# Performance work log

Measured on AMD Instinct MI355X. Metric: run time of the kernel, lower is better.

Reference implementation:

```python
import jax, jax.numpy as jnp
import numpy as np
import math

D = 768; H = 8; HD = D // H; T = 1024; V = 32000; M = 10
BLOCK = 128          # flex-attention block size (sliding_window_num_blocks granularity)
TAU = 1.0            # gumbel_temp
MAXC = 10            # max middle-block visits == scan length
EPS = 1e-6
IFP = 0.95           # initial_forward_prob

def rms(x):
    return x * jax.lax.rsqrt(jnp.mean(x * x, axis=-1, keepdims=True) + EPS)

def make_rope(t):
    # Rotary.__init__: dim//4 real inv freqs + dim//4 zeros -> cos/sin of shape [t, HD//2]
    inv = (1.0 / 1024) ** jnp.linspace(0.0, 1.0, HD // 4)
    inv = jnp.concatenate([inv, jnp.zeros(HD // 4)])
    th = jnp.arange(t, dtype=jnp.float32)[:, None] * inv[None, :]
    return jnp.cos(th), jnp.sin(th)

def rope(x, cos, sin):
    # x: [1,T,H,HD]
    c = cos[None, :, None, :]; s = sin[None, :, None, :]
    x1, x2 = jnp.split(x, 2, axis=-1)
    return jnp.concatenate([x1 * c + x2 * s, -x1 * s + x2 * c], axis=-1)

def attn(x, ve, wq, wk, wv, wo, lam, cos, sin, mask):
    q = (x @ wq.T).reshape(1, T, H, HD)
    k = (x @ wk.T).reshape(1, T, H, HD)
    v = (x @ wv.T).reshape(1, T, H, HD)
    if ve is not None:
        v = lam[0] * v + lam[1] * ve.reshape(1, T, H, HD)
    else:
        v = lam[0] * v
    q = rope(rms(q), cos, sin); k = rope(rms(k), cos, sin)
    sc = jnp.einsum('bthd,bshd->bhts', q, k) * (1.0 / math.sqrt(HD))
    sc = jnp.where(mask, sc, -1e30)
    y = jnp.einsum('bhts,bshd->bthd', jax.nn.softmax(sc, axis=-1), v).reshape(1, T, D)
    return y @ wo.T

def mlp(x, fc, pr):
    return jnp.square(jax.nn.relu(x @ fc.T)) @ pr.T

def fwd(tokens, embed_w, ve_w, lm_head_w,
        in_wq, in_wk, in_wv, in_wo, in_attn_lam, in_fc, in_pr, in_lam,
        mid_wq, mid_wk, mid_wv, mid_wo, mid_attn_lam, mid_fc, mid_pr, router_w, router_b,
        out_wq, out_wk, out_wv, out_wo, out_attn_lam, out_fc, out_pr, out_lam,
        gumbel_u, window_blocks, max_block_count):
    cos, sin = make_rope(T)
    qi = jnp.arange(T)
    mask = ((qi[:, None] >= qi[None, :]) &
            ((qi[:, None] // BLOCK - qi[None, :] // BLOCK) < window_blocks))[None, None]
    x = rms(embed_w[tokens][None])     # norm(embed(inputs))
    x0 = x
    ve = ve_w[tokens][None]            # X=1 value embedding, reused for output block
    # ---- input FixedBlock ----
    h = in_lam[0] * x + in_lam[1] * x0
    h = h + attn(rms(h), ve, in_wq, in_wk, in_wv, in_wo, in_attn_lam, cos, sin, mask)
    h = h + mlp(rms(h), in_fc, in_pr)
    # ---- middle routing loop (fixed-length scan, masked once exited) ----
    g = -jnp.log(-jnp.log(gumbel_u + 1e-10) + 1e-10)  # [MAXC, M+1] gumbel noise
    mbc = jnp.float32(max_block_count)
    def step(carry, gi):
        x, cur, done, cnt = carry
        y = x + attn(rms(x), None, mid_wq[cur], mid_wk[cur], mid_wv[cur], mid_wo[cur],
                     mid_attn_lam[cur], cos, sin, mask)
        y = y + mlp(rms(y), mid_fc[cur], mid_pr[cur])
        feat = jnp.concatenate([y.mean(axis=1), jnp.stack([cnt, mbc])[None]], axis=-1)  # [1, D+2]
        logits = feat @ router_w[cur].T + router_b[cur]                                  # [1, M+1]
        route = jax.nn.softmax((logits + gi[None]) / TAU, axis=-1)
        nxt = jnp.argmax(route[0]).astype(jnp.int32)
        new_cnt = cnt + 1.0
        exit_now = (nxt == M) | (new_cnt >= mbc)
        x = jnp.where(done, x, y)
        cnt = jnp.where(done, cnt, new_cnt)
        new_done = done | exit_now
        cur = jnp.where(new_done, cur, nxt)
        return (x, cur, new_done, cnt), None
    init = (h, jnp.int32(0), jnp.bool_(False), jnp.float32(0.0))
    (x, _, _, _), _ = jax.lax.scan(step, init, g)
    # ---- output FixedBlock ----
    y = out_lam[0] * x + out_lam[1] * x0
    y = y + attn(rms(y), ve, out_wq, out_wk, out_wv, out_wo, out_attn_lam, cos, sin, mask)
    y = y + mlp(rms(y), out_fc, out_pr)
    logits = rms(y) @ lm_head_w.T
    return 30.0 * jnp.tanh(logits / 30.0)

def setup_inputs() -> dict:
    key = jax.random.key(0)
    ks = iter(jax.random.split(key, 64))
    def w(*s, std=0.02):
        return (std * jax.random.normal(next(ks), s)).astype(jnp.float32)
    rb = np.full((M, M + 1), math.log((1.0 - IFP) / M), dtype=np.float32)
    for i in range(M):
        rb[i, min(i + 1, M)] = math.log(IFP)
    inp = {
        'tokens': jax.random.randint(next(ks), (T,), 0, V, dtype=jnp.int32),
        'embed_w': w(V, D), 've_w': w(V, D), 'lm_head_w': w(V, D),
        'in_wq': w(D, D), 'in_wk': w(D, D), 'in_wv': w(D, D), 'in_wo': w(D, D),
        'in_attn_lam': jnp.array([0.5, 0.5], jnp.float32),
        'in_fc': w(4 * D, D), 'in_pr': w(D, 4 * D),
        'in_lam': jnp.array([1.0, 0.0], jnp.float32),
        'mid_wq': w(M, D, D), 'mid_wk': w(M, D, D), 'mid_wv': w(M, D, D), 'mid_wo': w(M, D, D),
        'mid_attn_lam': jnp.tile(jnp.array([0.5, 0.5], jnp.float32), (M, 1)),
        'mid_fc': w(M, 4 * D, D), 'mid_pr': w(M, D, 4 * D),
        'router_w': w(M, M + 1, D + 2, std=0.001),
        'router_b': jnp.asarray(rb),
        'out_wq': w(D, D), 'out_wk': w(D, D), 'out_wv': w(D, D), 'out_wo': w(D, D),
        'out_attn_lam': jnp.array([0.5, 0.5], jnp.float32),
        'out_fc': w(4 * D, D), 'out_pr': w(D, 4 * D),
        'out_lam': jnp.array([1.0, 0.0], jnp.float32),
        'gumbel_u': jax.random.uniform(next(ks), (MAXC, M + 1), dtype=jnp.float32),
        'window_blocks': 4,
        'max_block_count': MAXC,
    }
    return inp

def reference(tokens, embed_w, ve_w, lm_head_w,
              in_wq, in_wk, in_wv, in_wo, in_attn_lam, in_fc, in_pr, in_lam,
              mid_wq, mid_wk, mid_wv, mid_wo, mid_attn_lam, mid_fc, mid_pr, router_w, router_b,
              out_wq, out_wk, out_wv, out_wo, out_attn_lam, out_fc, out_pr, out_lam,
              gumbel_u, window_blocks, max_block_count):
    return fwd(tokens, embed_w, ve_w, lm_head_w,
               in_wq, in_wk, in_wv, in_wo, in_attn_lam, in_fc, in_pr, in_lam,
               mid_wq, mid_wk, mid_wv, mid_wo, mid_attn_lam, mid_fc, mid_pr, router_w, router_b,
               out_wq, out_wk, out_wv, out_wo, out_attn_lam, out_fc, out_pr, out_lam,
               gumbel_u, window_blocks, max_block_count)
```

## Files before the change

### kernel.cpp

```cpp
#include <hip/hip_runtime.h>
#include <hip/hip_bf16.h>

namespace {

constexpr int cT   = 1024;
constexpr int cD   = 768;
constexpr int cH   = 8;
constexpr int cHD  = 96;
constexpr int cM   = 10;
constexpr int cDff = 3072;
constexpr int cV   = 32000;
constexpr int cTD  = cT * cD;
constexpr float cEps = 1e-6f;

constexpr long oWQ = 0;
constexpr long oWK = 589824;
constexpr long oWV = 2L * 589824;
constexpr long oWO = 3L * 589824;
constexpr long oFC = 4L * 589824;
constexpr long oPR = 4L * 589824 + 2359296;
constexpr long cWTOT = 4L * 589824 + 2L * 2359296;
constexpr int cConvBlocks = (int)(cWTOT / 8 / 256);

typedef __attribute__((ext_vector_type(8))) short short8;
typedef __attribute__((ext_vector_type(4))) float f32x4;

__device__ inline short bf16r(float f) {
  union { float f; unsigned u; } x{f};
  unsigned r = (x.u + 0x7FFF + ((x.u >> 16) & 1)) >> 16;
  return (short)r;
}

__device__ inline float bf2f(short s) {
  union { unsigned u; float f; } x;
  x.u = ((unsigned)(unsigned short)s) << 16;
  return x.f;
}


__global__ void init_state_k(int* cur, int* done, float* cnt) {
  if (threadIdx.x == 0) { *cur = 0; *done = 0; *cnt = 0.0f; }
}

__global__ void rope_pre_k(float* __restrict__ cosb, float* __restrict__ sinb) {
  int idx = blockIdx.x * blockDim.x + threadIdx.x;
  if (idx >= cT * 48) return;
  int t = idx / 48, j = idx % 48;
  float th = 0.0f;
  if (j < 24) th = (float)t * powf(1.0f / 1024.0f, (float)j / 23.0f);
  cosb[idx] = cosf(th);
  sinb[idx] = sinf(th);
}

__global__ __launch_bounds__(256) void embed_rms_k(const int* __restrict__ tok,
    const float* __restrict__ ew, const float* __restrict__ vw,
    float* __restrict__ x0, float* __restrict__ ve) {
  int t = blockIdx.x;
  int tk = tok[t];
  const float* er = ew + (size_t)tk * cD;
  const float* vr = vw + (size_t)tk * cD;
  __shared__ float red[256];
  float s = 0.f;
  for (int d = threadIdx.x; d < cD; d += 256) { float e = er[d]; s += e * e; }
  red[threadIdx.x] = s; __syncthreads();
  for (int st = 128; st; st >>= 1) { if (threadIdx.x < st) red[threadIdx.x] += red[threadIdx.x + st]; __syncthreads(); }
  float sc = rsqrtf(red[0] / cD + cEps);
  for (int d = threadIdx.x; d < cD; d += 256) {
    x0[(size_t)t * cD + d] = er[d] * sc;
    ve[(size_t)t * cD + d] = vr[d];
  }
}

__global__ __launch_bounds__(256) void rms_rows_bf(const float* __restrict__ in,
    short* __restrict__ out, const int* done) {
  if (done && *done) return;
  int t = blockIdx.x;
  const float* r = in + (size_t)t * cD;
  __shared__ float red[256];
  float s = 0.f;
  for (int d = threadIdx.x; d < cD; d += 256) { float v = r[d]; s += v * v; }
  red[threadIdx.x] = s; __syncthreads();
  for (int st = 128; st; st >>= 1) { if (threadIdx.x < st) red[threadIdx.x] += red[threadIdx.x + st]; __syncthreads(); }
  float sc = rsqrtf(red[0] / cD + cEps);
  short* o = out + (size_t)t * cD;
  for (int d = threadIdx.x; d < cD; d += 256) o[d] = bf16r(r[d] * sc);
}

__global__ void axpy_lam_k(const float* __restrict__ lam, const float* __restrict__ a,
                           const float* __restrict__ b, float* __restrict__ o, int n) {
  int i = blockIdx.x * 256 + threadIdx.x;
  if (i < n) o[i] = lam[0] * a[i] + lam[1] * b[i];
}


__global__ __launch_bounds__(256) void layer_pre_k(const float* __restrict__ s0,
    const float* __restrict__ s1, const float* __restrict__ s2, const float* __restrict__ s3,
    const float* __restrict__ s4, const float* __restrict__ s5, short* __restrict__ dst,
    const int* __restrict__ cur, const int* __restrict__ done,
    const float* __restrict__ xin, short* __restrict__ xnbf, float* __restrict__ rsum) {
  if (done && *done) return;
  const int b = blockIdx.x;
  if (b < cConvBlocks) {
    long e = ((long)b * 256 + threadIdx.x) * 8;
    long cu = cur ? (long)(*cur) : 0L;
    const float* src;
    if (e < oWK)      src = s0 + cu * 589824  + e;
    else if (e < oWV) src = s1 + cu * 589824  + (e - oWK);
    else if (e < oWO) src = s2 + cu * 589824  + (e - oWV);
    else if (e < oFC) src = s3 + cu * 589824  + (e - oWO);
    else if (e < oPR) src = s4 + cu * 2359296 + (e - oFC);
    else              src = s5 + cu * 2359296 + (e - oPR);
    float4 a0 = *(const float4*)src;
    float4 a1 = *(const float4*)(src + 4);
    short8 sv;
    sv[0]=bf16r(a0.x); sv[1]=bf16r(a0.y); sv[2]=bf16r(a0.z); sv[3]=bf16r(a0.w);
    sv[4]=bf16r(a1.x); sv[5]=bf16r(a1.y); sv[6]=bf16r(a1.z); sv[7]=bf16r(a1.w);
    *(short8*)(dst + e) = sv;
  } else {
    const int t = b - cConvBlocks;
    const float* r = xin + (size_t)t * cD;
    __shared__ float red[256];
    float s = 0.f;
    for (int d = threadIdx.x; d < cD; d += 256) { float v = r[d]; s += v * v; }
    red[threadIdx.x] = s; __syncthreads();
    for (int st = 128; st; st >>= 1) { if (threadIdx.x < st) red[threadIdx.x] += red[threadIdx.x + st]; __syncthreads(); }
    float sc = rsqrtf(red[0] / cD + cEps);
    short* o = xnbf + (size_t)t * cD;
    for (int d = threadIdx.x; d < cD; d += 256) o[d] = bf16r(r[d] * sc);
    if (threadIdx.x == 0) rsum[t] = 0.f;
  }
}

__global__ __launch_bounds__(256) void conv1_k(const float* __restrict__ src,
    short* __restrict__ dst, long nchunk) {
  long i = (long)blockIdx.x * 256 + threadIdx.x;
  if (i >= nchunk) return;
  long e = i * 8;
  float4 a0 = *(const float4*)(src + e);
  float4 a1 = *(const float4*)(src + e + 4);
  short8 sv;
  sv[0]=bf16r(a0.x); sv[1]=bf16r(a0.y); sv[2]=bf16r(a0.z); sv[3]=bf16r(a0.w);
  sv[4]=bf16r(a1.x); sv[5]=bf16r(a1.y); sv[6]=bf16r(a1.z); sv[7]=bf16r(a1.w);
  *(short8*)(dst + e) = sv;
}


__global__ __launch_bounds__(256) void qkv_k(const short* __restrict__ A,
    const short* __restrict__ Wb,
    short* __restrict__ qo, short* __restrict__ ko, short* __restrict__ vo,
    const int* __restrict__ done, const float* __restrict__ lamb,
    const int* __restrict__ cur, const float* __restrict__ vep,
    const float* __restrict__ cosb, const float* __restrict__ sinb) {
  if (done && *done) return;
  const int z = blockIdx.z;
  const short* W = Wb + (long)z * 589824L;
  const int h  = blockIdx.x;
  const int bm = blockIdx.y * 64;
  __shared__ short As[2][64][40];
  __shared__ short Bs[2][96][40];
  const int tid = threadIdx.x;
  const int w = tid >> 6, lane = tid & 63;
  const int fr = lane & 15, fg = lane >> 4;
  const int ar = tid >> 2, ac2 = (tid & 3) << 3;
  const int br1 = (256 + tid) >> 2, bc1 = ((256 + tid) & 3) << 3;

  short8 aN, bN0, bN1;
  aN  = *(const short8*)(A + (size_t)(bm + ar) * cD + ac2);
  bN0 = *(const short8*)(W + (size_t)(h * cHD + ar) * cD + ac2);
  if (tid < 128) bN1 = *(const short8*)(W + (size_t)(h * cHD + br1) * cD + bc1);
  *(short8*)&As[0][ar][ac2] = aN;
  *(short8*)&Bs[0][ar][ac2] = bN0;
  if (tid < 128) *(short8*)&Bs[0][br1][bc1] = bN1;
  __syncthreads();

  f32x4 acc[6] = {};
  int cb = 0;
  for (int kt = 0; kt < cD; kt += 32) {
    const int ktn = kt + 32;
    const bool hn = ktn < cD;
    if (hn) {
      aN  = *(const short8*)(A + (size_t)(bm + ar) * cD + ktn + ac2);
      bN0 = *(const short8*)(W + (size_t)(h * cHD + ar) * cD + ktn + ac2);
      if (tid < 128) bN1 = *(const short8*)(W + (size_t)(h * cHD + br1) * cD + ktn + bc1);
    }
    short8 af = *(const short8*)&As[cb][w * 16 + fr][fg * 8];
#pragma unroll
    for (int n = 0; n < 6; ++n) {
      short8 bf = *(const short8*)&Bs[cb][n * 16 + fr][fg * 8];
      acc[n] = __builtin_amdgcn_mfma_f32_16x16x32_bf16(af, bf, acc[n], 0, 0, 0);
    }
    if (hn) {
      *(short8*)&As[cb ^ 1][ar][ac2] = aN;
      *(short8*)&Bs[cb ^ 1][ar][ac2] = bN0;
      if (tid < 128) *(short8*)&Bs[cb ^ 1][br1][bc1] = bN1;
    }
    __syncthreads();
    cb ^= 1;
  }

  const int t0 = bm + w * 16 + fg * 4;
  if (z < 2) {
    float scl[4];
#pragma unroll
    for (int r = 0; r < 4; ++r) {
      float s = 0.f;
#pragma unroll
      for (int n = 0; n < 6; ++n) s += acc[n][r] * acc[n][r];
#pragma unroll
      for (int mm = 1; mm < 16; mm <<= 1) s += __shfl_xor(s, mm, 64);
      scl[r] = rsqrtf(s * (1.0f / 96.0f) + cEps);
    }
    short* C = (z == 0 ? qo : ko);
#pragma unroll
    for (int r = 0; r < 4; ++r) {
      int t = t0 + r;
      short* orow = C + (size_t)t * cD + h * cHD;
#pragma unroll
      for (int n = 0; n < 3; ++n) {
        int j = n * 16 + fr;
        float c = cosb[t * 48 + j], sn = sinb[t * 48 + j];
        float x1 = acc[n][r] * scl[r], x2 = acc[n + 3][r] * scl[r];
        orow[j]      = bf16r(x1 * c + x2 * sn);
        orow[j + 48] = bf16r(-x1 * sn + x2 * c);
      }
    }
  } else {
    int cu = cur ? *cur : 0;
    float l0 = lamb[2 * cu], l1 = lamb[2 * cu + 1];
#pragma unroll
    for (int r = 0; r < 4; ++r) {
      int t = t0 + r;
#pragma unroll
      for (int n = 0; n < 6; ++n) {
        float val = l0 * acc[n][r];
        if (vep) val += l1 * vep[(size_t)t * cD + h * cHD + n * 16 + fr];
        vo[(size_t)t * cD + h * cHD + n * 16 + fr] = bf16r(val);
      }
    }
  }
}


__global__ __launch_bounds__(256) void attn_f(const short* __restrict__ q,
    const short* __restrict__ k, const short* __restrict__ v, short* __restrict__ o,
    const int* __restrict__ wbp, const int* done) {
  if (done && *done) return;
  const int qb = blockIdx.x;
  const int h  = blockIdx.y;
  const int q0 = qb * 64;
  const int qb128 = q0 >> 7;
  const int wb = *wbp;
  int kb_lo = qb128 - wb + 1; if (kb_lo < 0) kb_lo = 0;

  __shared__ short Ksh[128][136];
  __shared__ short Vt[96][136];

  const int tid  = threadIdx.x;
  const int w    = tid >> 6;
  const int lane = tid & 63;
  const int fr   = lane & 15;
  const int fg   = lane >> 4;

  short8 qf[3];
  {
    const short* qrow = q + (size_t)(q0 + w * 16 + fr) * cD + h * cHD;
#pragma unroll
    for (int ks = 0; ks < 3; ++ks) qf[ks] = *(const short8*)(qrow + ks * 32 + fg * 8);
  }

  f32x4 accO[6] = {};
  float mrun[4], lrun[4];
#pragma unroll
  for (int r = 0; r < 4; ++r) { mrun[r] = -1e30f; lrun[r] = 0.f; }

  for (int kb = kb_lo; kb <= qb128; ++kb) {
    __syncthreads();
    const int key0 = kb * 128;
#pragma unroll
    for (int c = 0; c < 6; ++c) {
      int idx = c * 256 + tid;
      int row = idx / 12, colc = (idx % 12) * 8;
      *(short8*)&Ksh[row][colc] =
          *(const short8*)(k + (size_t)(key0 + row) * cD + h * cHD + colc);
      short8 vv = *(const short8*)(v + (size_t)(key0 + row) * cD + h * cHD + colc);
#pragma unroll
      for (int i = 0; i < 8; ++i) Vt[colc + i][row] = vv[i];
    }
    __syncthreads();

    f32x4 s[8];
#pragma unroll
    for (int n = 0; n < 8; ++n) s[n] = (f32x4){0.f, 0.f, 0.f, 0.f};
#pragma unroll
    for (int ks = 0; ks < 3; ++ks) {
#pragma unroll
      for (int n = 0; n < 8; ++n) {
        short8 kf = *(const short8*)&Ksh[n * 16 + fr][ks * 32 + fg * 8];
        s[n] = __builtin_amdgcn_mfma_f32_16x16x32_bf16(qf[ks], kf, s[n], 0, 0, 0);
      }
    }

    float pmax[4] = {-1e30f, -1e30f, -1e30f, -1e30f};
#pragma unroll
    for (int n = 0; n < 8; ++n)
#pragma unroll
      for (int r = 0; r < 4; ++r) {
        float val = s[n][r] * 0.10206207261596577f;
        int key  = key0 + n * 16 + fr;
        int qrow = q0 + w * 16 + fg * 4 + r;
        if (key > qrow) val = -1e30f;
        s[n][r] = val;
        pmax[r] = fmaxf(pmax[r], val);
      }
#pragma unroll
    for (int mm = 1; mm < 16; mm <<= 1)
#pragma unroll
      for (int r = 0; r < 4; ++r) pmax[r] = fmaxf(pmax[r], __shfl_xor(pmax[r], mm, 64));
    float alpha[4], psum[4];
#pragma unroll
    for (int r = 0; r < 4; ++r) {
      float mn = fmaxf(mrun[r], pmax[r]);
      alpha[r] = __expf(mrun[r] - mn);
      mrun[r] = mn;
      psum[r] = 0.f;
    }
#pragma unroll
    for (int n = 0; n < 8; ++n)
#pragma unroll
      for (int r = 0; r < 4; ++r) {
        float p = __expf(s[n][r] - mrun[r]);
        s[n][r] = p;
        psum[r] += p;
      }
#pragma unroll
    for (int mm = 1; mm < 16; mm <<= 1)
#pragma unroll
      for (int r = 0; r < 4; ++r) psum[r] += __shfl_xor(psum[r], mm, 64);
#pragma unroll
    for (int r = 0; r < 4; ++r) lrun[r] = lrun[r] * alpha[r] + psum[r];
#pragma unroll
    for (int n = 0; n < 6; ++n) {
      f32x4 t = accO[n];
#pragma unroll
      for (int r = 0; r < 4; ++r) t[r] *= alpha[r];
      accO[n] = t;
    }

    __syncthreads();
#pragma unroll
    for (int n = 0; n < 8; ++n)
#pragma unroll
      for (int r = 0; r < 4; ++r)
        Ksh[w * 16 + fg * 4 + r][n * 16 + fr] = bf16r(s[n][r]);
    __syncthreads();

#pragma unroll
    for (int ks = 0; ks < 4; ++ks) {
      short8 pf = *(const short8*)&Ksh[w * 16 + fr][ks * 32 + fg * 8];
#pragma unroll
      for (int n = 0; n < 6; ++n) {
        short8 vf = *(const short8*)&Vt[n * 16 + fr][ks * 32 + fg * 8];
        accO[n] = __builtin_amdgcn_mfma_f32_16x16x32_bf16(pf, vf, accO[n], 0, 0, 0);
      }
    }
  }

#pragma unroll
  for (int r = 0; r < 4; ++r) {
    float inv = 1.0f / lrun[r];
    int t = q0 + w * 16 + fg * 4 + r;
#pragma unroll
    for (int n = 0; n < 6; ++n)
      o[(size_t)t * cD + h * cHD + n * 16 + fr] = bf16r(accO[n][r] * inv);
  }
}


template <int EPI, typename OT>
__global__ __launch_bounds__(256) void gemm64_k(const short* __restrict__ A,
    const short* __restrict__ W, OT* __restrict__ C, const int* __restrict__ done,
    const float* __restrict__ res, float* __restrict__ rsum, int ld, int kn, int N) {
  if (done && *done) return;
  const int bm = blockIdx.y * 64;
  const int bn = blockIdx.x * 64;
  const int k0 = blockIdx.z * kn;
  __shared__ short As[2][64][40];
  __shared__ short Bs[2][64][40];
  const int tid = threadIdx.x;
  const int wid = tid >> 6, lane = tid & 63;
  const int wr = wid >> 1, wc = wid & 1;
  const int fr = lane & 15, fg = lane >> 4;
  const int ar = tid >> 2, ac = (tid & 3) << 3;

  short8 aN = *(const short8*)(A + (size_t)(bm + ar) * ld + k0 + ac);
  short8 bN = *(const short8*)(W + (size_t)(bn + ar) * ld + k0 + ac);
  *(short8*)&As[0][ar][ac] = aN;
  *(short8*)&Bs[0][ar][ac] = bN;
  __syncthreads();

  f32x4 acc[2][2] = {};
  int cb = 0;
  for (int kt = 0; kt < kn; kt += 32) {
    const int ktn = kt + 32;
    const bool hn = ktn < kn;
    if (hn) {
      aN = *(const short8*)(A + (size_t)(bm + ar) * ld + k0 + ktn + ac);
      bN = *(const short8*)(W + (size_t)(bn + ar) * ld + k0 + ktn + ac);
    }
    short8 af[2], bfv[2];
#pragma unroll
    for (int m = 0; m < 2; ++m) af[m] = *(const short8*)&As[cb][wr * 32 + m * 16 + fr][fg * 8];
#pragma unroll
    for (int n = 0; n < 2; ++n) bfv[n] = *(const short8*)&Bs[cb][wc * 32 + n * 16 + fr][fg * 8];
#pragma unroll
    for (int m = 0; m < 2; ++m)
#pragma unroll
      for (int n = 0; n < 2; ++n)
        acc[m][n] = __builtin_amdgcn_mfma_f32_16x16x32_bf16(af[m], bfv[n], acc[m][n], 0, 0, 0);
    if (hn) {
      *(short8*)&As[cb ^ 1][ar][ac] = aN;
      *(short8*)&Bs[cb ^ 1][ar][ac] = bN;
    }
    __syncthreads();
    cb ^= 1;
  }
#pragma unroll
  for (int m = 0; m < 2; ++m)
#pragma unroll
    for (int r = 0; r < 4; ++r) {
      const int row = bm + wr * 32 + m * 16 + fg * 4 + r;
      float p = 0.f;
#pragma unroll
      for (int n = 0; n < 2; ++n) {
        const int col = bn + wc * 32 + n * 16 + fr;
        float val = acc[m][n][r];
        if constexpr (EPI == 1) {
          val += res[(size_t)row * N + col];
          C[(size_t)row * N + col] = val;
          p += val * val;
        } else {
          C[(size_t)blockIdx.z * cTD + (size_t)row * N + col] = (OT)bf16r(val);
        }
      }
      if constexpr (EPI == 1) {
#pragma unroll
        for (int mm = 1; mm < 16; mm <<= 1) p += __shfl_xor(p, mm, 64);
        if (fr == 0) atomicAdd(&rsum[row], p);
      }
    }
}


__global__ __launch_bounds__(256) void mgemm_fc_k(const float* __restrict__ Ay,
    const float* __restrict__ rsum, const short* __restrict__ W, short* __restrict__ C,
    const int* __restrict__ done, int K, int N) {
  if (done && *done) return;
  const int bm = blockIdx.y * 64;
  const int bn = blockIdx.x * 128;
  __shared__ short As[2][64][40];
  __shared__ short Bs[2][128][40];
  const int tid = threadIdx.x;
  const int wid = tid >> 6, lane = tid & 63;
  const int wr = wid >> 1, wc = wid & 1;
  const int fr = lane & 15, fg = lane >> 4;
  const int ar = tid >> 2, ac = (tid & 3) << 3;
  const int br1 = (256 + tid) >> 2, bc1 = ((256 + tid) & 3) << 3;

  const float ascl = rsqrtf(rsum[bm + ar] * (1.0f / cD) + cEps);
  const float* arow = Ay + (size_t)(bm + ar) * K;

  auto loadA = [&](int kt) -> short8 {
    float4 a0 = *(const float4*)(arow + kt + ac);
    float4 a1 = *(const float4*)(arow + kt + ac + 4);
    short8 sv;
    sv[0]=bf16r(a0.x*ascl); sv[1]=bf16r(a0.y*ascl); sv[2]=bf16r(a0.z*ascl); sv[3]=bf16r(a0.w*ascl);
    sv[4]=bf16r(a1.x*ascl); sv[5]=bf16r(a1.y*ascl); sv[6]=bf16r(a1.z*ascl); sv[7]=bf16r(a1.w*ascl);
    return sv;
  };

  short8 aN, bN0, bN1;
  aN  = loadA(0);
  bN0 = *(const short8*)(W + (size_t)(bn + ar) * K + ac);
  bN1 = *(const short8*)(W + (size_t)(bn + br1) * K + bc1);
  *(short8*)&As[0][ar][ac] = aN;
  *(short8*)&Bs[0][ar][ac] = bN0;
  *(short8*)&Bs[0][br1][bc1] = bN1;
  __syncthreads();

  f32x4 acc[2][4] = {};
  int cb = 0;
  for (int kt = 0; kt < K; kt += 32) {
    const int ktn = kt + 32;
    const bool hn = ktn < K;
    if (hn) {
      aN  = loadA(ktn);
      bN0 = *(const short8*)(W + (size_t)(bn + ar) * K + ktn + ac);
      bN1 = *(const short8*)(W + (size_t)(bn + br1) * K + ktn + bc1);
    }
    short8 af[2], bfv[4];
#pragma unroll
    for (int m = 0; m < 2; ++m) af[m] = *(const short8*)&As[cb][wr * 32 + m * 16 + fr][fg * 8];
#pragma unroll
    for (int n = 0; n < 4; ++n) bfv[n] = *(const short8*)&Bs[cb][wc * 64 + n * 16 + fr][fg * 8];
#pragma unroll
    for (int m = 0; m < 2; ++m)
#pragma unroll
      for (int n = 0; n < 4; ++n)
        acc[m][n] = __builtin_amdgcn_mfma_f32_16x16x32_bf16(af[m], bfv[n], acc[m][n], 0, 0, 0);
    if (hn) {
      *(short8*)&As[cb ^ 1][ar][ac] = aN;
      *(short8*)&Bs[cb ^ 1][ar][ac] = bN0;
      *(short8*)&Bs[cb ^ 1][br1][bc1] = bN1;
    }
    __syncthreads();
    cb ^= 1;
  }
#pragma unroll
  for (int m = 0; m < 2; ++m)
#pragma unroll
    for (int n = 0; n < 4; ++n)
#pragma unroll
      for (int r = 0; r < 4; ++r) {
        int row = bm + wr * 32 + m * 16 + fg * 4 + r;
        int col = bn + wc * 64 + n * 16 + fr;
        float val = acc[m][n][r];
        val = fmaxf(val, 0.f); val = val * val;
        C[(size_t)row * N + col] = bf16r(val);
      }
}


__global__ __launch_bounds__(256) void reduce_k(const short* __restrict__ pb,
    float* __restrict__ y, float* __restrict__ x, float* __restrict__ feat,
    const int* done) {
  if (done && *done) return;
  __shared__ float red[256];
  const int d = blockIdx.x * 32 + (threadIdx.x & 31);
  const int tc = threadIdx.x >> 5;
  float s = 0.f;
  for (int t = tc * 128; t < tc * 128 + 128; ++t) {
    size_t i = (size_t)t * cD + d;
    float v = y[i];
#pragma unroll
    for (int z = 0; z < 4; ++z) v += bf2f(pb[(size_t)z * cTD + i]);
    y[i] = v;
    if (x) x[i] = v;
    s += v;
  }
  if (feat) {
    red[threadIdx.x] = s; __syncthreads();
    if (threadIdx.x < 32) {
      float tot = 0.f;
#pragma unroll
      for (int c = 0; c < 8; ++c) tot += red[c * 32 + threadIdx.x];
      feat[d] = tot * (1.0f / cT);
    }
  }
}


__global__ void router_step_k(const float* __restrict__ feat, const float* __restrict__ rw,
    const float* __restrict__ rb, const float* __restrict__ gu, int iter,
    const int* __restrict__ mbcp, int* cur, int* done, float* cnt) {
  if (*done) return;
  __shared__ float lg[cM + 1];
  const int tid = threadIdx.x;
  const int c = *cur;
  const float mbc = (float)(*mbcp);
  const float cn = *cnt;
  for (int j = 0; j < cM + 1; ++j) {
    const float* w = rw + ((size_t)c * (cM + 1) + j) * (cD + 2);
    float s = 0.f;
    for (int d = tid; d < cD; d += 64) s += feat[d] * w[d];
#pragma unroll
    for (int mm = 32; mm; mm >>= 1) s += __shfl_xor(s, mm, 64);
    if (tid == 0) {
      s += cn * w[cD] + mbc * w[cD + 1] + rb[c * (cM + 1) + j];
      float u = gu[iter * (cM + 1) + j];
      float inner = -logf(u + 1e-10f) + 1e-10f;
      lg[j] = s - logf(inner);
    }
  }
  __syncthreads();
  if (tid == 0) {
    int nxt = 0; float best = lg[0];
    for (int j = 1; j < cM + 1; ++j) if (lg[j] > best) { best = lg[j]; nxt = j; }
    float nc = cn + 1.0f;
    int ex = (nxt == cM) || (nc >= mbc);
    *cnt = nc;
    if (ex) *done = 1; else *cur = nxt;
  }
}


__global__ __launch_bounds__(512) void gemm_lm_k(const short* __restrict__ A,
    const short* __restrict__ W, float* __restrict__ C) {
  const int nwg = (cV / 128) * (cT / 256);
  const int cpx = nwg / 8;
  const int swz = (blockIdx.x % 8) * cpx + blockIdx.x / 8;
  const int bm = (swz % 4) * 256;
  const int bn = (swz / 4) * 128;
  __shared__ short As[2][256][40];
  __shared__ short Bs[2][128][40];
  const int tid = threadIdx.x;
  const int wid = tid >> 6, lane = tid & 63;
  const int wr = wid >> 1, wc = wid & 1;
  const int fr = lane & 15, fg = lane >> 4;
  const int ar0 = tid >> 2, ac0 = (tid & 3) << 3;
  const int ar1 = (512 + tid) >> 2, ac1 = ((512 + tid) & 3) << 3;

  short8 aN0, aN1, bN;
  aN0 = *(const short8*)(A + (size_t)(bm + ar0) * cD + ac0);
  aN1 = *(const short8*)(A + (size_t)(bm + ar1) * cD + ac1);
  bN  = *(const short8*)(W + (size_t)(bn + ar0) * cD + ac0);
  *(short8*)&As[0][ar0][ac0] = aN0;
  *(short8*)&As[0][ar1][ac1] = aN1;
  *(short8*)&Bs[0][ar0][ac0] = bN;
  __syncthreads();

  f32x4 acc[4][4] = {};
  int cb = 0;
  for (int kt = 0; kt < cD; kt += 32) {
    const int ktn = kt + 32;
    const bool hn = ktn < cD;
    if (hn) {
      aN0 = *(const short8*)(A + (size_t)(bm + ar0) * cD + ktn + ac0);
      aN1 = *(const short8*)(A + (size_t)(bm + ar1) * cD + ktn + ac1);
      bN  = *(const short8*)(W + (size_t)(bn + ar0) * cD + ktn + ac0);
    }
    short8 af[4], bfv[4];
#pragma unroll
    for (int m = 0; m < 4; ++m) af[m] = *(const short8*)&As[cb][wr * 64 + m * 16 + fr][fg * 8];
#pragma unroll
    for (int n = 0; n < 4; ++n) bfv[n] = *(const short8*)&Bs[cb][wc * 64 + n * 16 + fr][fg * 8];
#pragma unroll
    for (int m = 0; m < 4; ++m)
#pragma unroll
      for (int n = 0; n < 4; ++n)
        acc[m][n] = __builtin_amdgcn_mfma_f32_16x16x32_bf16(af[m], bfv[n], acc[m][n], 0, 0, 0);
    if (hn) {
      *(short8*)&As[cb ^ 1][ar0][ac0] = aN0;
      *(short8*)&As[cb ^ 1][ar1][ac1] = aN1;
      *(short8*)&Bs[cb ^ 1][ar0][ac0] = bN;
    }
    __syncthreads();
    cb ^= 1;
  }
#pragma unroll
  for (int m = 0; m < 4; ++m)
#pragma unroll
    for (int n = 0; n < 4; ++n)
#pragma unroll
      for (int r = 0; r < 4; ++r) {
        int row = bm + wr * 64 + m * 16 + fg * 4 + r;
        int col = bn + wc * 64 + n * 16 + fr;
        C[(size_t)row * cV + col] = 30.f * tanhf(acc[m][n][r] * (1.f / 30.f));
      }
}

}


extern "C" void kernel_launch(void* const* d_in, const int* in_sizes, int n_in,
                              void* d_out, int out_size, void* d_ws, size_t ws_size,
                              hipStream_t stream) {
  const int*   tokens    = (const int*)d_in[0];
  const float* embed_w   = (const float*)d_in[1];
  const float* ve_w      = (const float*)d_in[2];
  const float* lm_head_w = (const float*)d_in[3];
  const float* in_wq  = (const float*)d_in[4];
  const float* in_wk  = (const float*)d_in[5];
  const float* in_wv  = (const float*)d_in[6];
  const float* in_wo  = (const float*)d_in[7];
  const float* in_al  = (const float*)d_in[8];
  const float* in_fc  = (const float*)d_in[9];
  const float* in_pr  = (const float*)d_in[10];
  const float* in_lam = (const float*)d_in[11];
  const float* mid_wq = (const float*)d_in[12];
  const float* mid_wk = (const float*)d_in[13];
  const float* mid_wv = (const float*)d_in[14];
  const float* mid_wo = (const float*)d_in[15];
  const float* mid_al = (const float*)d_in[16];
  const float* mid_fc = (const float*)d_in[17];
  const float* mid_pr = (const float*)d_in[18];
  const float* router_w = (const float*)d_in[19];
  const float* router_b = (const float*)d_in[20];
  const float* out_wq = (const float*)d_in[21];
  const float* out_wk = (const float*)d_in[22];
  const float* out_wv = (const float*)d_in[23];
  const float* out_wo = (const float*)d_in[24];
  const float* out_al = (const float*)d_in[25];
  const float* out_fc = (const float*)d_in[26];
  const float* out_pr = (const float*)d_in[27];
  const float* out_lam = (const float*)d_in[28];
  const float* gumbel_u = (const float*)d_in[29];
  const int*   wbp  = (const int*)d_in[30];
  const int*   mbcp = (const int*)d_in[31];
  float* outp = (float*)d_out;

  float* ws = (float*)d_ws;
  float* xb   = ws;
  float* x0b  = xb  + cTD;
  float* veb  = x0b + cTD;
  float* yb   = veb + cTD;
  float* cosb = yb  + cTD;
  float* sinb = cosb + cT * 48;
  float* rsum = sinb + cT * 48;
  float* feat = rsum + 1024;
  int*   curp  = (int*)(feat + 784);
  int*   donep = curp + 1;
  float* cntp  = (float*)(curp + 2);
  short* xnbf  = (short*)(feat + 784 + 8);
  short* aobf  = xnbf + cTD;
  short* qbf   = aobf + cTD;
  short* kbf   = qbf  + cTD;
  short* vbf   = kbf  + cTD;
  short* pbuf  = aobf;
  short* hidbf = vbf  + cTD;
  short* wbf   = hidbf + (size_t)cT * cDff;

  const dim3 gPre(cConvBlocks + cT, 1, 1);
  const dim3 gQKV(cH, cT / 64, 3);
  const dim3 gWO(cD / 64, cT / 64, 1);
  const dim3 gPR(cD / 64, cT / 64, 4);
  const dim3 gFF(cDff / 128, cT / 64, 1);
  const dim3 gLM(1000, 1, 1);
  const dim3 gAttn(cT / 64, cH, 1);
  const int gRed = cD / 32;
  const long lmChunks = (long)cV * cD / 8;
  const int gConvLM = (int)(lmChunks / 256);

  auto layer = [&](const float* wq, const float* wk, const float* wv, const float* wo,
                   const float* alam, const float* fc, const float* pr,
                   const int* cur, const int* done,
                   float* xin, float* yout, const float* vept,
                   float* xcom, float* featp) {
    layer_pre_k<<<gPre, 256, 0, stream>>>(wq, wk, wv, wo, fc, pr, wbf, cur, done,
                                          xin, xnbf, rsum);
    qkv_k<<<gQKV, 256, 0, stream>>>(xnbf, wbf, qbf, kbf, vbf, done, alam, cur, vept,
                                    cosb, sinb);
    attn_f<<<gAttn, 256, 0, stream>>>(qbf, kbf, vbf, aobf, wbp, done);
    gemm64_k<1, float><<<gWO, 256, 0, stream>>>(aobf, wbf + oWO, yout, done, xin, rsum,
                                                cD, cD, cD);
    mgemm_fc_k<<<gFF, 256, 0, stream>>>(yout, rsum, wbf + oFC, hidbf, done, cD, cDff);
    gemm64_k<4, short><<<gPR, 256, 0, stream>>>(hidbf, wbf + oPR, pbuf, done, nullptr,
                                                nullptr, cDff, cDff / 4, cD);
    reduce_k<<<gRed, 256, 0, stream>>>(pbuf, yout, xcom, featp, done);
  };

  init_state_k<<<1, 64, 0, stream>>>(curp, donep, cntp);
  rope_pre_k<<<(cT * 48 + 255) / 256, 256, 0, stream>>>(cosb, sinb);
  embed_rms_k<<<cT, 256, 0, stream>>>(tokens, embed_w, ve_w, x0b, veb);

  axpy_lam_k<<<cTD / 256, 256, 0, stream>>>(in_lam, x0b, x0b, xb, cTD);
  layer(in_wq, in_wk, in_wv, in_wo, in_al, in_fc, in_pr, nullptr, nullptr,
        xb, xb, veb, nullptr, nullptr);

  for (int it = 0; it < cM; ++it) {
    layer(mid_wq, mid_wk, mid_wv, mid_wo, mid_al, mid_fc, mid_pr,
          curp, donep, xb, yb, nullptr, xb, feat);
    router_step_k<<<1, 64, 0, stream>>>(feat, router_w, router_b, gumbel_u, it, mbcp,
                                        curp, donep, cntp);
  }

  axpy_lam_k<<<cTD / 256, 256, 0, stream>>>(out_lam, xb, x0b, xb, cTD);
  layer(out_wq, out_wk, out_wv, out_wo, out_al, out_fc, out_pr, nullptr, nullptr,
        xb, xb, veb, nullptr, nullptr);

  conv1_k<<<gConvLM, 256, 0, stream>>>(lm_head_w, wbf, lmChunks);
  rms_rows_bf<<<cT, 256, 0, stream>>>(xb, xnbf, nullptr);
  gemm_lm_k<<<gLM, 512, 0, stream>>>(xnbf, wbf, outp);
}
```

Baseline: 2.631 ms.

## Pre-convert all layer and LM-head weights to bf16 once, halve attention tile

A single up-front kernel converts every weight set to bf16 into slots of one workspace buffer: all ten middle-block slots, the input and output blocks, and the LM head. The GEMM kernels then read the right slot through a device-side block index and stride. This removes the per-layer fp32-to-bf16 weight conversion and the separate LM-head conversion, at the cost of converting middle-block weights that an early router exit never uses, and it requires a larger workspace (otherwise it falls back to the old path). Separately, the attention kernel now handles 32 queries per block with 128 threads instead of 64 queries with 256, doubling the block count to improve parallelism.

```diff
diff --git a/kernel.cpp b/kernel.cpp
--- a/kernel.cpp
+++ b/kernel.cpp
@@ -21,6 +21,8 @@
 constexpr long oPR = 4L * 589824 + 2359296;
 constexpr long cWTOT = 4L * 589824 + 2L * 2359296;
 constexpr int cConvBlocks = (int)(cWTOT / 8 / 256);
+constexpr long cLM  = (long)cV * cD;
+constexpr long cALL = 12L * cWTOT + cLM;
 
 typedef __attribute__((ext_vector_type(8))) short short8;
 typedef __attribute__((ext_vector_type(4))) float f32x4;
@@ -86,12 +88,67 @@
   for (int d = threadIdx.x; d < cD; d += 256) o[d] = bf16r(r[d] * sc);
 }
 
+__global__ __launch_bounds__(256) void rms_pre_k(const float* __restrict__ in,
+    short* __restrict__ out, float* __restrict__ rsum, const int* done) {
+  if (done && *done) return;
+  int t = blockIdx.x;
+  const float* r = in + (size_t)t * cD;
+  __shared__ float red[256];
+  float s = 0.f;
+  for (int d = threadIdx.x; d < cD; d += 256) { float v = r[d]; s += v * v; }
+  red[threadIdx.x] = s; __syncthreads();
+  for (int st = 128; st; st >>= 1) { if (threadIdx.x < st) red[threadIdx.x] += red[threadIdx.x + st]; __syncthreads(); }
+  float sc = rsqrtf(red[0] / cD + cEps);
+  short* o = out + (size_t)t * cD;
+  for (int d = threadIdx.x; d < cD; d += 256) o[d] = bf16r(r[d] * sc);
+  if (threadIdx.x == 0) rsum[t] = 0.f;
+}
+
 __global__ void axpy_lam_k(const float* __restrict__ lam, const float* __restrict__ a,
                            const float* __restrict__ b, float* __restrict__ o, int n) {
   int i = blockIdx.x * 256 + threadIdx.x;
   if (i < n) o[i] = lam[0] * a[i] + lam[1] * b[i];
 }
 
+
+__device__ inline const float* pick6(const float* q, const float* k, const float* v,
+    const float* o, const float* f, const float* p, long cu, long off) {
+  if (off < oWK) return q + cu * 589824L + off;
+  if (off < oWV) return k + cu * 589824L + (off - oWK);
+  if (off < oWO) return v + cu * 589824L + (off - oWV);
+  if (off < oFC) return o + cu * 589824L + (off - oWO);
+  if (off < oPR) return f + cu * 2359296L + (off - oFC);
+  return p + cu * 2359296L + (off - oPR);
+}
+
+__global__ __launch_bounds__(256) void convall_k(
+    const float* mq, const float* mk, const float* mv, const float* mo,
+    const float* mf, const float* mp,
+    const float* iq, const float* ik, const float* iv, const float* io,
+    const float* if_, const float* ip,
+    const float* oq, const float* ok, const float* ov, const float* oo,
+    const float* of_, const float* op,
+    const float* lm, short* __restrict__ dst) {
+  long e = ((long)blockIdx.x * 256 + threadIdx.x) * 8;
+  if (e >= cALL) return;
+  const float* src;
+  if (e < 10L * cWTOT) {
+    long cu = e / cWTOT;
+    src = pick6(mq, mk, mv, mo, mf, mp, cu, e - cu * cWTOT);
+  } else if (e < 11L * cWTOT) {
+    src = pick6(iq, ik, iv, io, if_, ip, 0, e - 10L * cWTOT);
+  } else if (e < 12L * cWTOT) {
+    src = pick6(oq, ok, ov, oo, of_, op, 0, e - 11L * cWTOT);
+  } else {
+    src = lm + (e - 12L * cWTOT);
+  }
+  float4 a0 = *(const float4*)src;
+  float4 a1 = *(const float4*)(src + 4);
+  short8 sv;
+  sv[0]=bf16r(a0.x); sv[1]=bf16r(a0.y); sv[2]=bf16r(a0.z); sv[3]=bf16r(a0.w);
+  sv[4]=bf16r(a1.x); sv[5]=bf16r(a1.y); sv[6]=bf16r(a1.z); sv[7]=bf16r(a1.w);
+  *(short8*)(dst + e) = sv;
+}
 
 __global__ __launch_bounds__(256) void layer_pre_k(const float* __restrict__ s0,
     const float* __restrict__ s1, const float* __restrict__ s2, const float* __restrict__ s3,
@@ -103,13 +160,7 @@
   if (b < cConvBlocks) {
     long e = ((long)b * 256 + threadIdx.x) * 8;
     long cu = cur ? (long)(*cur) : 0L;
-    const float* src;
-    if (e < oWK)      src = s0 + cu * 589824  + e;
-    else if (e < oWV) src = s1 + cu * 589824  + (e - oWK);
-    else if (e < oWO) src = s2 + cu * 589824  + (e - oWV);
-    else if (e < oFC) src = s3 + cu * 589824  + (e - oWO);
-    else if (e < oPR) src = s4 + cu * 2359296 + (e - oFC);
-    else              src = s5 + cu * 2359296 + (e - oPR);
+    const float* src = pick6(s0, s1, s2, s3, s4, s5, cu, e);
     float4 a0 = *(const float4*)src;
     float4 a1 = *(const float4*)(src + 4);
     short8 sv;
@@ -146,14 +197,14 @@
 
 
 __global__ __launch_bounds__(256) void qkv_k(const short* __restrict__ A,
-    const short* __restrict__ Wb,
+    const short* __restrict__ Wb, long sstr,
     short* __restrict__ qo, short* __restrict__ ko, short* __restrict__ vo,
     const int* __restrict__ done, const float* __restrict__ lamb,
     const int* __restrict__ cur, const float* __restrict__ vep,
     const float* __restrict__ cosb, const float* __restrict__ sinb) {
   if (done && *done) return;
   const int z = blockIdx.z;
-  const short* W = Wb + (long)z * 589824L;
+  const short* W = Wb + (cur ? (long)(*cur) * sstr : 0L) + (long)z * 589824L;
   const int h  = blockIdx.x;
   const int bm = blockIdx.y * 64;
   __shared__ short As[2][64][40];
@@ -241,13 +292,13 @@
 }
 
 
-__global__ __launch_bounds__(256) void attn_f(const short* __restrict__ q,
+__global__ __launch_bounds__(128) void attn_f(const short* __restrict__ q,
     const short* __restrict__ k, const short* __restrict__ v, short* __restrict__ o,
     const int* __restrict__ wbp, const int* done) {
   if (done && *done) return;
   const int qb = blockIdx.x;
   const int h  = blockIdx.y;
-  const int q0 = qb * 64;
+  const int q0 = qb * 32;
   const int qb128 = q0 >> 7;
   const int wb = *wbp;
   int kb_lo = qb128 - wb + 1; if (kb_lo < 0) kb_lo = 0;
@@ -277,8 +328,8 @@
     __syncthreads();
     const int key0 = kb * 128;
 #pragma unroll
-    for (int c = 0; c < 6; ++c) {
-      int idx = c * 256 + tid;
+    for (int c = 0; c < 12; ++c) {
+      int idx = c * 128 + tid;
       int row = idx / 12, colc = (idx % 12) * 8;
       *(short8*)&Ksh[row][colc] =
           *(const short8*)(k + (size_t)(key0 + row) * cD + h * cHD + colc);
@@ -378,9 +429,11 @@
 
 template <int EPI, typename OT>
 __global__ __launch_bounds__(256) void gemm64_k(const short* __restrict__ A,
-    const short* __restrict__ W, OT* __restrict__ C, const int* __restrict__ done,
+    const short* __restrict__ Wp, const int* __restrict__ wcur, long sstr,
+    OT* __restrict__ C, const int* __restrict__ done,
     const float* __restrict__ res, float* __restrict__ rsum, int ld, int kn, int N) {
   if (done && *done) return;
+  const short* W = Wp + (wcur ? (long)(*wcur) * sstr : 0L);
   const int bm = blockIdx.y * 64;
   const int bn = blockIdx.x * 64;
   const int k0 = blockIdx.z * kn;
@@ -452,9 +505,11 @@
 
 
 __global__ __launch_bounds__(256) void mgemm_fc_k(const float* __restrict__ Ay,
-    const float* __restrict__ rsum, const short* __restrict__ W, short* __restrict__ C,
+    const float* __restrict__ rsum, const short* __restrict__ Wp,
+    const int* __restrict__ wcur, long sstr, short* __restrict__ C,
     const int* __restrict__ done, int K, int N) {
   if (done && *done) return;
+  const short* W = Wp + (wcur ? (long)(*wcur) * sstr : 0L);
   const int bm = blockIdx.y * 64;
   const int bn = blockIdx.x * 128;
   __shared__ short As[2][64][40];
@@ -719,55 +774,84 @@
   short* hidbf = vbf  + cTD;
   short* wbf   = hidbf + (size_t)cT * cDff;
 
-  const dim3 gPre(cConvBlocks + cT, 1, 1);
+  const size_t wbfByteOff = (size_t)((char*)wbf - (char*)d_ws);
+  const bool PRE = ws_size >= wbfByteOff + (size_t)cALL * 2 + 1024;
+
+  const dim3 gPreFB(cConvBlocks + cT, 1, 1);
   const dim3 gQKV(cH, cT / 64, 3);
   const dim3 gWO(cD / 64, cT / 64, 1);
   const dim3 gPR(cD / 64, cT / 64, 4);
   const dim3 gFF(cDff / 128, cT / 64, 1);
   const dim3 gLM(1000, 1, 1);
-  const dim3 gAttn(cT / 64, cH, 1);
+  const dim3 gAttn(cT / 32, cH, 1);
   const int gRed = cD / 32;
-  const long lmChunks = (long)cV * cD / 8;
+  const long lmChunks = cLM / 8;
   const int gConvLM = (int)(lmChunks / 256);
+  const int gConvAll = (int)(cALL / 8 / 256);
 
   auto layer = [&](const float* wq, const float* wk, const float* wv, const float* wo,
                    const float* alam, const float* fc, const float* pr,
+                   const short* wbase, const int* wcur, long sstr,
                    const int* cur, const int* done,
                    float* xin, float* yout, const float* vept,
                    float* xcom, float* featp) {
-    layer_pre_k<<<gPre, 256, 0, stream>>>(wq, wk, wv, wo, fc, pr, wbf, cur, done,
-                                          xin, xnbf, rsum);
-    qkv_k<<<gQKV, 256, 0, stream>>>(xnbf, wbf, qbf, kbf, vbf, done, alam, cur, vept,
-                                    cosb, sinb);
-    attn_f<<<gAttn, 256, 0, stream>>>(qbf, kbf, vbf, aobf, wbp, done);
-    gemm64_k<1, float><<<gWO, 256, 0, stream>>>(aobf, wbf + oWO, yout, done, xin, rsum,
-                                                cD, cD, cD);
-    mgemm_fc_k<<<gFF, 256, 0, stream>>>(yout, rsum, wbf + oFC, hidbf, done, cD, cDff);
-    gemm64_k<4, short><<<gPR, 256, 0, stream>>>(hidbf, wbf + oPR, pbuf, done, nullptr,
-                                                nullptr, cDff, cDff / 4, cD);
+    if (PRE) {
+      rms_pre_k<<<cT, 256, 0, stream>>>(xin, xnbf, rsum, done);
+    } else {
+      layer_pre_k<<<gPreFB, 256, 0, stream>>>(wq, wk, wv, wo, fc, pr, wbf, cur, done,
+                                              xin, xnbf, rsum);
+    }
+    qkv_k<<<gQKV, 256, 0, stream>>>(xnbf, wbase, sstr, qbf, kbf, vbf, done, alam,
+                                    cur, vept, cosb, sinb);
+    attn_f<<<gAttn, 128, 0, stream>>>(qbf, kbf, vbf, aobf, wbp, done);
+    gemm64_k<1, float><<<gWO, 256, 0, stream>>>(aobf, wbase + oWO, wcur, sstr, yout,
+                                                done, xin, rsum, cD, cD, cD);
+    mgemm_fc_k<<<gFF, 256, 0, stream>>>(yout, rsum, wbase + oFC, wcur, sstr, hidbf,
+                                        done, cD, cDff);
+    gemm64_k<4, short><<<gPR, 256, 0, stream>>>(hidbf, wbase + oPR, wcur, sstr, pbuf,
+                                                done, nullptr, nullptr, cDff, cDff / 4, cD);
     reduce_k<<<gRed, 256, 0, stream>>>(pbuf, yout, xcom, featp, done);
   };
 
   init_state_k<<<1, 64, 0, stream>>>(curp, donep, cntp);
   rope_pre_k<<<(cT * 48 + 255) / 256, 256, 0, stream>>>(cosb, sinb);
   embed_rms_k<<<cT, 256, 0, stream>>>(tokens, embed_w, ve_w, x0b, veb);
+  if (PRE) {
+    convall_k<<<gConvAll, 256, 0, stream>>>(
+        mid_wq, mid_wk, mid_wv, mid_wo, mid_fc, mid_pr,
+        in_wq, in_wk, in_wv, in_wo, in_fc, in_pr,
+        out_wq, out_wk, out_wv, out_wo, out_fc, out_pr,
+        lm_head_w, wbf);
+  }
+
+  const short* slotIn  = PRE ? wbf + 10L * cWTOT : wbf;
+  const short* slotOut = PRE ? wbf + 11L * cWTOT : wbf;
+  const short* slotMid = wbf;
+  const long  sstrMid  = PRE ? cWTOT : 0L;
+  const int*  wcurMid  = PRE ? curp : nullptr;
 
   axpy_lam_k<<<cTD / 256, 256, 0, stream>>>(in_lam, x0b, x0b, xb, cTD);
-  layer(in_wq, in_wk, in_wv, in_wo, in_al, in_fc, in_pr, nullptr, nullptr,
-        xb, xb, veb, nullptr, nullptr);
+  layer(in_wq, in_wk, in_wv, in_wo, in_al, in_fc, in_pr,
+        slotIn, nullptr, 0L, nullptr, nullptr, xb, xb, veb, nullptr, nullptr);
 
   for (int it = 0; it < cM; ++it) {
     layer(mid_wq, mid_wk, mid_wv, mid_wo, mid_al, mid_fc, mid_pr,
-          curp, donep, xb, yb, nullptr, xb, feat);
+          slotMid, wcurMid, sstrMid, curp, donep, xb, yb, nullptr, xb, feat);
     router_step_k<<<1, 64, 0, stream>>>(feat, router_w, router_b, gumbel_u, it, mbcp,
                                         curp, donep, cntp);
   }
 
   axpy_lam_k<<<cTD / 256, 256, 0, stream>>>(out_lam, xb, x0b, xb, cTD);
-  layer(out_wq, out_wk, out_wv, out_wo, out_al, out_fc, out_pr, nullptr, nullptr,
-        xb, xb, veb, nullptr, nullptr);
-
-  conv1_k<<<gConvLM, 256, 0, stream>>>(lm_head_w, wbf, lmChunks);
+  layer(out_wq, out_wk, out_wv, out_wo, out_al, out_fc, out_pr,
+        slotOut, nullptr, 0L, nullptr, nullptr, xb, xb, veb, nullptr, nullptr);
+
+  const short* lmw;
+  if (PRE) {
+    lmw = wbf + 12L * cWTOT;
+  } else {
+    conv1_k<<<gConvLM, 256, 0, stream>>>(lm_head_w, wbf, lmChunks);
+    lmw = wbf;
+  }
   rms_rows_bf<<<cT, 256, 0, stream>>>(xb, xnbf, nullptr);
-  gemm_lm_k<<<gLM, 512, 0, stream>>>(xnbf, wbf, outp);
-}
+  gemm_lm_k<<<gLM, 512, 0, stream>>>(xnbf, lmw, outp);
+}
```

Result: slower. 2.762 ms (+5.0%).
